# Optimization experiments

Measured on AMD Instinct MI355X. Metric: run time of the kernel, lower is better.

The kernel has to match this reference:

```python
import jax, jax.numpy as jnp
import numpy as np

B, S, H = 2, 2048, 768
NH, DH = 12, 64  # num_heads, dim_head; inner_dim = NH*DH = H
SCALE = DH ** -0.5


def setup_inputs() -> dict:
    key = jax.random.key(0)
    k1, k2, k3 = jax.random.split(key, 3)
    x = jax.random.normal(k1, (B, S, H), dtype=jnp.float32)
    w_qkv = jax.random.normal(k2, (3 * NH * DH, H), dtype=jnp.float32) * (H ** -0.5)
    w_out = jax.random.normal(k3, (H, NH * DH), dtype=jnp.float32) * ((NH * DH) ** -0.5)
    b_out = jnp.zeros((H,), dtype=jnp.float32)
    return {"x": x, "w_qkv": w_qkv, "w_out": w_out, "b_out": b_out}


def reference(x, w_qkv, w_out, b_out):
    b, s, _ = x.shape
    # qkv linear: [b, s, 3*inner]
    qkv = jnp.einsum('bsh,oh->bso', x, w_qkv)
    # 'b s (qkv l d) -> qkv b l s d'  (l = heads)
    qkv = qkv.reshape(b, s, 3, NH, DH).transpose(2, 0, 3, 1, 4)
    q, k, v = qkv[0], qkv[1], qkv[2]  # each [b, nh, s, dh]
    att = jax.nn.softmax(jnp.einsum('bhxd,bhyd->bhxy', q, k) * SCALE, axis=-1)
    out = jnp.einsum('bhxy,bhyd->bhxd', att, v)  # [b, nh, s, dh]
    out = out.transpose(0, 2, 1, 3).reshape(b, s, NH * DH)  # 'b h l d -> b l (h d)'
    return jnp.einsum('bsi,oi->bso', out, w_out) + b_out
```

## Files before the change

kernel.cpp:

```cpp
#include <hip/hip_runtime.h>
#include <cstdint>
#include <cstddef>

typedef __bf16 bf16;
typedef __bf16 bf16x8 __attribute__((ext_vector_type(8)));
typedef __bf16 bf16x4 __attribute__((ext_vector_type(4)));
typedef float  f32x4  __attribute__((ext_vector_type(4)));
typedef float  f32x16 __attribute__((ext_vector_type(16)));

constexpr int Bb  = 2;
constexpr int Ss  = 2048;
constexpr int Hh  = 768;
constexpr int NHh = 12;
constexpr int DHh = 64;
constexpr int Mm  = Bb * Ss;
constexpr int N3  = 3 * Hh;
constexpr int QKW = 2 * Hh;

__device__ __forceinline__ float fexp2(float x) { return __builtin_amdgcn_exp2f(x); }

__device__ __forceinline__ void gload_lds16(void* lds, const void* g) {
  __builtin_amdgcn_global_load_lds(
      (__attribute__((address_space(1))) void*)(uintptr_t)g,
      (__attribute__((address_space(3))) void*)(uint32_t)(uintptr_t)lds,
      16, 0, 0);
}

__global__ void cvt3_f32_bf16(const float* __restrict__ x,  bf16* __restrict__ xb,
                              const float* __restrict__ w1, bf16* __restrict__ w1b,
                              const float* __restrict__ w2, bf16* __restrict__ w2b) {
  const int st = gridDim.x * blockDim.x;
  int i0 = blockIdx.x * blockDim.x + threadIdx.x;
  for (int i = i0; i < 786432; i += st) {
    float4 v = ((const float4*)x)[i];
    bf16x4 o; o[0]=(bf16)v.x; o[1]=(bf16)v.y; o[2]=(bf16)v.z; o[3]=(bf16)v.w;
    ((bf16x4*)xb)[i] = o;
  }
  for (int i = i0; i < 442368; i += st) {
    float4 v = ((const float4*)w1)[i];
    bf16x4 o; o[0]=(bf16)v.x; o[1]=(bf16)v.y; o[2]=(bf16)v.z; o[3]=(bf16)v.w;
    ((bf16x4*)w1b)[i] = o;
  }
  for (int i = i0; i < 147456; i += st) {
    float4 v = ((const float4*)w2)[i];
    bf16x4 o; o[0]=(bf16)v.x; o[1]=(bf16)v.y; o[2]=(bf16)v.z; o[3]=(bf16)v.w;
    ((bf16x4*)w2b)[i] = o;
  }
}

template<int CSTRIDE, int OUTMODE, int BM>
__global__ __launch_bounds__(256, 2)
void gemm_bt(const bf16* __restrict__ A, const bf16* __restrict__ Bw,
             bf16* __restrict__ Cb, bf16* __restrict__ VtG,
             float* __restrict__ Cf, const float* __restrict__ bias)
{
  constexpr int K = 768;
  constexpr int NT = K / 32;
  constexpr int MI = BM / 32;
  constexpr int ABUF = BM * 64;
  __shared__ bf16 As[2][BM * 32];
  __shared__ bf16 Bs[2][128 * 32];
  const int tid  = threadIdx.x;
  const int wid  = tid >> 6, lane = tid & 63;
  const int lr   = lane & 15, lk = lane >> 4;
  const int n0   = blockIdx.x * 128, m0 = blockIdx.y * BM;
  const int wm   = (wid >> 1) * (BM / 2), wn = (wid & 1) * 64;

  f32x4 acc[MI][4] = {};

  const char* Ag = (const char*)(A  + (size_t)m0 * K) + (size_t)(tid >> 2) * (K * 2) + (tid & 3) * 16;
  const char* Bg = (const char*)(Bw + (size_t)n0 * K) + (size_t)(tid >> 2) * (K * 2) + (tid & 3) * 16;
  constexpr size_t rstep = (size_t)64 * K * 2;

  auto stage = [&](int buf, int kb) {
    char* aw = (char*)As + buf * ABUF + wid * 1024;
    char* bw = (char*)Bs + buf * 8192 + wid * 1024;
    gload_lds16(aw, Ag + (size_t)kb * 2);
    if constexpr (BM == 128)
      gload_lds16(aw + 4096, Ag + rstep + (size_t)kb * 2);
    gload_lds16(bw,        Bg + (size_t)kb * 2);
    gload_lds16(bw + 4096, Bg + rstep + (size_t)kb * 2);
  };

  stage(0, 0);
  asm volatile("s_waitcnt vmcnt(0)" ::: "memory");
  __syncthreads();

#pragma unroll 1
  for (int t = 0; t < NT; ++t) {
    const int cur = t & 1;
    if (t + 1 < NT) stage(cur ^ 1, (t + 1) * 32);
    __builtin_amdgcn_sched_barrier(0);

    bf16x8 af[MI], bfv[4];
#pragma unroll
    for (int i = 0; i < MI; ++i)
      af[i]  = *(const bf16x8*)((const char*)As + cur * ABUF + ((wm + i * 16 + lr) * 32 + lk * 8) * 2);
#pragma unroll
    for (int j = 0; j < 4; ++j)
      bfv[j] = *(const bf16x8*)((const char*)Bs + cur * 8192 + ((wn + j * 16 + lr) * 32 + lk * 8) * 2);
#pragma unroll
    for (int i = 0; i < MI; ++i)
#pragma unroll
      for (int j = 0; j < 4; ++j)
        acc[i][j] = __builtin_amdgcn_mfma_f32_16x16x32_bf16(af[i], bfv[j], acc[i][j], 0, 0, 0);

    __syncthreads();
  }

  if constexpr (OUTMODE == 1) {
#pragma unroll
    for (int i = 0; i < MI; ++i)
#pragma unroll
      for (int j = 0; j < 4; ++j) {
        const int n = n0 + wn + j * 16 + lr;
        const float bv = bias[n];
#pragma unroll
        for (int r = 0; r < 4; ++r) {
          const int m = m0 + wm + i * 16 + lk * 4 + r;
          Cf[(size_t)m * CSTRIDE + n] = acc[i][j][r] + bv;
        }
      }
  } else {
    if (n0 < QKW) {
#pragma unroll
      for (int i = 0; i < MI; ++i)
#pragma unroll
        for (int j = 0; j < 4; ++j) {
          const int n = n0 + wn + j * 16 + lr;
#pragma unroll
          for (int r = 0; r < 4; ++r) {
            const int m = m0 + wm + i * 16 + lk * 4 + r;
            Cb[(size_t)m * CSTRIDE + n] = (bf16)acc[i][j][r];
          }
        }
    } else {
      const int bidx = m0 >> 11;
      const int s0 = (m0 & 2047) + wm + lk * 4;
#pragma unroll
      for (int i = 0; i < MI; ++i)
#pragma unroll
        for (int j = 0; j < 4; ++j) {
          const int colv = (n0 - QKW) + wn + j * 16 + lr;
          const int hh = colv >> 6, dd = colv & 63;
          const int bh = bidx * NHh + hh;
          const int mb = s0 + i * 16;
          bf16x4 pv;
#pragma unroll
          for (int r = 0; r < 4; ++r) pv[r] = (bf16)acc[i][j][r];
          const size_t idx8 = (((size_t)bh * 128 + (mb >> 4)) * 2 + (dd >> 5)) * 64
                              + ((mb >> 3) & 1) * 32 + (dd & 31);
          *(bf16x4*)(VtG + idx8 * 8 + (mb & 7)) = pv;
        }
    }
  }
}

__global__ __launch_bounds__(256, 3)
void attn_fwd5(const bf16* __restrict__ qk, const bf16* __restrict__ Vfrag,
               bf16* __restrict__ aout)
{
  __shared__ __align__(16) char lds[32768];
  const int tid  = threadIdx.x;
  const int wid  = tid >> 6, lane = tid & 63;
  const int lq   = lane & 31, hi = lane >> 5;
  const int qh   = wid & 1, grp = wid >> 1;

  const int orig = blockIdx.x;
  const int swz  = (orig & 7) * 96 + (orig >> 3);
  const int qb   = swz & 31;
  const int bh   = swz >> 5;
  const int b    = bh / NHh, h = bh % NHh;
  const int q0   = qb * 64 + qh * 32;
  const int kvbase = grp * 1024;

  constexpr float Cs = 0.18033688011112042f;
  const bf16* qrow = qk + (size_t)(b * Ss + q0 + lq) * QKW + h * DHh;
  bf16x8 qf[4];
#pragma unroll
  for (int j = 0; j < 4; ++j) {
    bf16x8 t = *(const bf16x8*)(qrow + j * 16 + hi * 8);
#pragma unroll
    for (int e = 0; e < 8; ++e) t[e] = (bf16)((float)t[e] * Cs);
    qf[j] = t;
  }

  const int strow = qh * 32 + (lane >> 3);
  const int stcol = ((lane & 7) * 16) ^ (((lane >> 3) & 7) << 4);
  const char* Kg0 = (const char*)(qk + (size_t)(b * Ss) * QKW + Hh + h * DHh)
                    + (size_t)strow * (QKW * 2) + stcol;
  auto stageK = [&](int buf, int kvt) {
    char* db = lds + grp * 16384 + buf * 8192 + qh * 4096;
    const char* sg = Kg0 + (size_t)kvt * (QKW * 2);
#pragma unroll
    for (int c = 0; c < 4; ++c)
      gload_lds16(db + c * 1024, sg + (size_t)(c * 8) * (QKW * 2));
  };

  const char* Vf = (const char*)Vfrag + (size_t)bh * 262144 + lane * 16;

  f32x16 oacc[2] = {};
  f32x16 lacc = {};
  bf16x8 ones;
#pragma unroll
  for (int e = 0; e < 8; ++e) ones[e] = (bf16)1.0f;

  stageK(0, kvbase);
  asm volatile("s_waitcnt vmcnt(0)" ::: "memory");
  __builtin_amdgcn_sched_barrier(0);

#pragma unroll 1
  for (int i = 0; i < 16; ++i) {
    const int cur = i & 1;

    __builtin_amdgcn_s_barrier();

    bf16x8 vf[4][2];
    {
      const char* vp = Vf + (size_t)(grp * 64 + i * 4) * 2048;
#pragma unroll
      for (int s = 0; s < 4; ++s)
#pragma unroll
        for (int dc = 0; dc < 2; ++dc)
          vf[s][dc] = *(const bf16x8*)(vp + (s * 2 + dc) * 1024);
    }

    stageK(cur ^ 1, kvbase + ((i + 1) & 15) * 64);
    __builtin_amdgcn_sched_barrier(0);

    f32x16 sacc[2];
    __builtin_amdgcn_s_setprio(1);
#pragma unroll
    for (int kvc = 0; kvc < 2; ++kvc) {
      f32x16 s = {};
      const int row = kvc * 32 + lq;
      const char* kb = lds + grp * 16384 + cur * 8192 + row * 128;
      const int sw = (lq & 7) << 4;
#pragma unroll
      for (int j = 0; j < 4; ++j) {
        bf16x8 kf = *(const bf16x8*)(kb + ((j * 32 + hi * 16) ^ sw));
        s = __builtin_amdgcn_mfma_f32_32x32x16_bf16(kf, qf[j], s, 0, 0, 0);
      }
      sacc[kvc] = s;
    }
    __builtin_amdgcn_s_setprio(0);

    uint32_t w[2][8];
#pragma unroll
    for (int kvc = 0; kvc < 2; ++kvc)
#pragma unroll
      for (int m = 0; m < 8; ++m) {
        union { bf16 hh[2]; uint32_t u; } cv;
        cv.hh[0] = (bf16)fexp2(sacc[kvc][2 * m]);
        cv.hh[1] = (bf16)fexp2(sacc[kvc][2 * m + 1]);
        w[kvc][m] = cv.u;
      }

    asm volatile("s_waitcnt vmcnt(4)" ::: "memory");
    __builtin_amdgcn_sched_barrier(0);

    __builtin_amdgcn_s_setprio(1);
#pragma unroll
    for (int s = 0; s < 4; ++s) {
      const int kvc = s >> 1, sb = s & 1;
      uint32_t a0 = w[kvc][4 * sb + 0], b0 = w[kvc][4 * sb + 2];
      uint32_t a1 = w[kvc][4 * sb + 1], b1 = w[kvc][4 * sb + 3];
      asm("v_permlane32_swap_b32 %0, %1" : "+v"(a0), "+v"(b0));
      asm("v_permlane32_swap_b32 %0, %1" : "+v"(a1), "+v"(b1));
      union { uint32_t u[4]; bf16x8 v; } pf;
      pf.u[0] = a0; pf.u[1] = a1; pf.u[2] = b0; pf.u[3] = b1;
#pragma unroll
      for (int dc = 0; dc < 2; ++dc)
        oacc[dc] = __builtin_amdgcn_mfma_f32_32x32x16_bf16(vf[s][dc], pf.v, oacc[dc], 0, 0, 0);
      lacc = __builtin_amdgcn_mfma_f32_32x32x16_bf16(ones, pf.v, lacc, 0, 0, 0);
    }
    __builtin_amdgcn_s_setprio(0);

    asm volatile("s_waitcnt vmcnt(0)" ::: "memory");
    __builtin_amdgcn_sched_barrier(0);
  }

  __syncthreads();

  if (grp == 1) {
    char* mb = lds + qh * 8704;
#pragma unroll
    for (int dc = 0; dc < 2; ++dc)
#pragma unroll
      for (int rr = 0; rr < 4; ++rr) {
        f32x4 t;
#pragma unroll
        for (int e = 0; e < 4; ++e) t[e] = oacc[dc][rr * 4 + e];
        *(f32x4*)(mb + (dc * 4 + rr) * 1024 + lane * 16) = t;
      }
    *(float*)(mb + 8192 + lane * 4) = lacc[0];
  }
  __syncthreads();
  if (grp == 0) {
    const char* mb = lds + qh * 8704;
    const float l2 = *(const float*)(mb + 8192 + lane * 4);
    const float linv = 1.0f / (lacc[0] + l2);
    bf16* orow = aout + (size_t)(b * Ss + q0 + lq) * Hh + h * DHh;
#pragma unroll
    for (int dc = 0; dc < 2; ++dc)
#pragma unroll
      for (int rr = 0; rr < 4; ++rr) {
        const f32x4 o2 = *(const f32x4*)(mb + (dc * 4 + rr) * 1024 + lane * 16);
        bf16x4 ov;
#pragma unroll
        for (int e = 0; e < 4; ++e)
          ov[e] = (bf16)((oacc[dc][rr * 4 + e] + o2[e]) * linv);
        *(bf16x4*)(orow + dc * 32 + rr * 8 + hi * 4) = ov;
      }
  }
}

extern "C" void kernel_launch(void* const* d_in, const int* in_sizes, int n_in,
                              void* d_out, int out_size, void* d_ws, size_t ws_size,
                              hipStream_t stream) {
  const float* x     = (const float*)d_in[0];
  const float* w_qkv = (const float*)d_in[1];
  const float* w_out = (const float*)d_in[2];
  const float* b_out = (const float*)d_in[3];
  char* ws = (char*)d_ws;
  bf16* xb    = (bf16*)(ws + 0);
  bf16* wqkvb = (bf16*)(ws + 6291456);
  bf16* woutb = (bf16*)(ws + 9830400);
  bf16* qkb   = (bf16*)(ws + 11010048);
  bf16* Vfrag = (bf16*)(ws + 23592960);
  bf16* aoutb = (bf16*)(ws + 29884416);

  cvt3_f32_bf16<<<2048, 256, 0, stream>>>(x, xb, w_qkv, wqkvb, w_out, woutb);

  gemm_bt<QKW, 0, 128><<<dim3(18, 32), 256, 0, stream>>>(xb, wqkvb, qkb, Vfrag, nullptr, nullptr);
  attn_fwd5<<<768, 256, 0, stream>>>(qkb, Vfrag, aoutb);
  gemm_bt<Hh, 1, 64><<<dim3(6, 64), 256, 0, stream>>>(aoutb, woutb, nullptr, nullptr,
                                                      (float*)d_out, b_out);
}
```

Measured before the change: 87.90 us.

## Write K in MFMA fragment layout and load K/V straight to registers

The QKV GEMM epilogue now writes K into a per-head fragment layout that matches the MFMA operand order, as was already done for V. This lets the attention kernel drop LDS staging and block barriers for K and load K and V fragments directly into registers, prefetching the next tile after the PV step. The row-sum now comes from adding the exp values in registers rather than from an extra MFMA against a ones vector. LDS use shrinks and launch bounds go up to 4 blocks per CU. The trade-offs are scattered 2-byte stores in the GEMM epilogue for K and more registers held live for the prefetched fragments.

```diff
diff --git a/kernel.cpp b/kernel.cpp
--- a/kernel.cpp
+++ b/kernel.cpp
@@ -48,10 +48,10 @@
   }
 }
 
-template<int CSTRIDE, int OUTMODE, int BM>
+template<int OUTMODE, int BM>
 __global__ __launch_bounds__(256, 2)
 void gemm_bt(const bf16* __restrict__ A, const bf16* __restrict__ Bw,
-             bf16* __restrict__ Cb, bf16* __restrict__ VtG,
+             bf16* __restrict__ Qb, bf16* __restrict__ Kf, bf16* __restrict__ Vf,
              float* __restrict__ Cf, const float* __restrict__ bias)
 {
   constexpr int K = 768;
@@ -118,11 +118,13 @@
 #pragma unroll
         for (int r = 0; r < 4; ++r) {
           const int m = m0 + wm + i * 16 + lk * 4 + r;
-          Cf[(size_t)m * CSTRIDE + n] = acc[i][j][r] + bv;
+          Cf[(size_t)m * Hh + n] = acc[i][j][r] + bv;
         }
       }
   } else {
-    if (n0 < QKW) {
+    const int bidx = m0 >> 11;
+    const int kvb  = (m0 & 2047) + wm + lk * 4;
+    if (n0 < Hh) {
 #pragma unroll
       for (int i = 0; i < MI; ++i)
 #pragma unroll
@@ -131,12 +133,26 @@
 #pragma unroll
           for (int r = 0; r < 4; ++r) {
             const int m = m0 + wm + i * 16 + lk * 4 + r;
-            Cb[(size_t)m * CSTRIDE + n] = (bf16)acc[i][j][r];
+            Qb[(size_t)m * Hh + n] = (bf16)acc[i][j][r];
+          }
+        }
+    } else if (n0 < QKW) {
+#pragma unroll
+      for (int i = 0; i < MI; ++i)
+#pragma unroll
+        for (int j = 0; j < 4; ++j) {
+          const int colv = (n0 - Hh) + wn + j * 16 + lr;
+          const int hh = colv >> 6, dd = colv & 63;
+          bf16* kfh = Kf + (size_t)(bidx * NHh + hh) * 131072;
+#pragma unroll
+          for (int r = 0; r < 4; ++r) {
+            const int kv = kvb + i * 16 + r;
+            const size_t idx = (size_t)((((kv >> 5) * 4 + (dd >> 4)) * 64
+                                + ((dd >> 3) & 1) * 32 + (kv & 31)) * 8 + (dd & 7));
+            kfh[idx] = (bf16)acc[i][j][r];
           }
         }
     } else {
-      const int bidx = m0 >> 11;
-      const int s0 = (m0 & 2047) + wm + lk * 4;
 #pragma unroll
       for (int i = 0; i < MI; ++i)
 #pragma unroll
@@ -144,23 +160,23 @@
           const int colv = (n0 - QKW) + wn + j * 16 + lr;
           const int hh = colv >> 6, dd = colv & 63;
           const int bh = bidx * NHh + hh;
-          const int mb = s0 + i * 16;
+          const int mb = kvb + i * 16;
           bf16x4 pv;
 #pragma unroll
           for (int r = 0; r < 4; ++r) pv[r] = (bf16)acc[i][j][r];
           const size_t idx8 = (((size_t)bh * 128 + (mb >> 4)) * 2 + (dd >> 5)) * 64
                               + ((mb >> 3) & 1) * 32 + (dd & 31);
-          *(bf16x4*)(VtG + idx8 * 8 + (mb & 7)) = pv;
+          *(bf16x4*)(Vf + idx8 * 8 + (mb & 7)) = pv;
         }
     }
   }
 }
 
-__global__ __launch_bounds__(256, 3)
-void attn_fwd5(const bf16* __restrict__ qk, const bf16* __restrict__ Vfrag,
-               bf16* __restrict__ aout)
+__global__ __launch_bounds__(256, 4)
+void attn_fwd6(const bf16* __restrict__ Qb, const bf16* __restrict__ Kfrag,
+               const bf16* __restrict__ Vfrag, bf16* __restrict__ aout)
 {
-  __shared__ __align__(16) char lds[32768];
+  __shared__ __align__(16) char lds[17408];
   const int tid  = threadIdx.x;
   const int wid  = tid >> 6, lane = tid & 63;
   const int lq   = lane & 31, hi = lane >> 5;
@@ -172,10 +188,9 @@
   const int bh   = swz >> 5;
   const int b    = bh / NHh, h = bh % NHh;
   const int q0   = qb * 64 + qh * 32;
-  const int kvbase = grp * 1024;
 
   constexpr float Cs = 0.18033688011112042f;
-  const bf16* qrow = qk + (size_t)(b * Ss + q0 + lq) * QKW + h * DHh;
+  const bf16* qrow = Qb + (size_t)(b * Ss + q0 + lq) * Hh + h * DHh;
   bf16x8 qf[4];
 #pragma unroll
   for (int j = 0; j < 4; ++j) {
@@ -185,47 +200,27 @@
     qf[j] = t;
   }
 
-  const int strow = qh * 32 + (lane >> 3);
-  const int stcol = ((lane & 7) * 16) ^ (((lane >> 3) & 7) << 4);
-  const char* Kg0 = (const char*)(qk + (size_t)(b * Ss) * QKW + Hh + h * DHh)
-                    + (size_t)strow * (QKW * 2) + stcol;
-  auto stageK = [&](int buf, int kvt) {
-    char* db = lds + grp * 16384 + buf * 8192 + qh * 4096;
-    const char* sg = Kg0 + (size_t)kvt * (QKW * 2);
-#pragma unroll
-    for (int c = 0; c < 4; ++c)
-      gload_lds16(db + c * 1024, sg + (size_t)(c * 8) * (QKW * 2));
-  };
-
-  const char* Vf = (const char*)Vfrag + (size_t)bh * 262144 + lane * 16;
+  const char* Kf = (const char*)Kfrag + (size_t)bh * 262144 + grp * 131072 + lane * 16;
+  const char* Vf = (const char*)Vfrag + (size_t)bh * 262144 + grp * 131072 + lane * 16;
 
   f32x16 oacc[2] = {};
-  f32x16 lacc = {};
-  bf16x8 ones;
-#pragma unroll
-  for (int e = 0; e < 8; ++e) ones[e] = (bf16)1.0f;
-
-  stageK(0, kvbase);
-  asm volatile("s_waitcnt vmcnt(0)" ::: "memory");
-  __builtin_amdgcn_sched_barrier(0);
+  float rsum = 0.f;
+
+  bf16x8 kf[2][4], vf[4][2];
+#pragma unroll
+  for (int kvc = 0; kvc < 2; ++kvc)
+#pragma unroll
+    for (int j = 0; j < 4; ++j)
+      kf[kvc][j] = *(const bf16x8*)(Kf + kvc * 4096 + j * 1024);
+#pragma unroll
+  for (int s4 = 0; s4 < 4; ++s4)
+#pragma unroll
+    for (int dc = 0; dc < 2; ++dc)
+      vf[s4][dc] = *(const bf16x8*)(Vf + (s4 * 2 + dc) * 1024);
 
 #pragma unroll 1
   for (int i = 0; i < 16; ++i) {
-    const int cur = i & 1;
-
-    __builtin_amdgcn_s_barrier();
-
-    bf16x8 vf[4][2];
-    {
-      const char* vp = Vf + (size_t)(grp * 64 + i * 4) * 2048;
-#pragma unroll
-      for (int s = 0; s < 4; ++s)
-#pragma unroll
-        for (int dc = 0; dc < 2; ++dc)
-          vf[s][dc] = *(const bf16x8*)(vp + (s * 2 + dc) * 1024);
-    }
-
-    stageK(cur ^ 1, kvbase + ((i + 1) & 15) * 64);
+    asm volatile("s_waitcnt vmcnt(8)" ::: "memory");
     __builtin_amdgcn_sched_barrier(0);
 
     f32x16 sacc[2];
@@ -233,36 +228,36 @@
 #pragma unroll
     for (int kvc = 0; kvc < 2; ++kvc) {
       f32x16 s = {};
-      const int row = kvc * 32 + lq;
-      const char* kb = lds + grp * 16384 + cur * 8192 + row * 128;
-      const int sw = (lq & 7) << 4;
-#pragma unroll
-      for (int j = 0; j < 4; ++j) {
-        bf16x8 kf = *(const bf16x8*)(kb + ((j * 32 + hi * 16) ^ sw));
-        s = __builtin_amdgcn_mfma_f32_32x32x16_bf16(kf, qf[j], s, 0, 0, 0);
-      }
+#pragma unroll
+      for (int j = 0; j < 4; ++j)
+        s = __builtin_amdgcn_mfma_f32_32x32x16_bf16(kf[kvc][j], qf[j], s, 0, 0, 0);
       sacc[kvc] = s;
     }
     __builtin_amdgcn_s_setprio(0);
+    __builtin_amdgcn_sched_barrier(0);
 
     uint32_t w[2][8];
+    float rp[4] = {0.f, 0.f, 0.f, 0.f};
 #pragma unroll
     for (int kvc = 0; kvc < 2; ++kvc)
 #pragma unroll
       for (int m = 0; m < 8; ++m) {
+        const float e0 = fexp2(sacc[kvc][2 * m]);
+        const float e1 = fexp2(sacc[kvc][2 * m + 1]);
+        rp[m & 3] += e0 + e1;
         union { bf16 hh[2]; uint32_t u; } cv;
-        cv.hh[0] = (bf16)fexp2(sacc[kvc][2 * m]);
-        cv.hh[1] = (bf16)fexp2(sacc[kvc][2 * m + 1]);
+        cv.hh[0] = (bf16)e0; cv.hh[1] = (bf16)e1;
         w[kvc][m] = cv.u;
       }
-
-    asm volatile("s_waitcnt vmcnt(4)" ::: "memory");
+    rsum += (rp[0] + rp[1]) + (rp[2] + rp[3]);
+
+    asm volatile("s_waitcnt vmcnt(0)" ::: "memory");
     __builtin_amdgcn_sched_barrier(0);
 
     __builtin_amdgcn_s_setprio(1);
 #pragma unroll
-    for (int s = 0; s < 4; ++s) {
-      const int kvc = s >> 1, sb = s & 1;
+    for (int s4 = 0; s4 < 4; ++s4) {
+      const int kvc = s4 >> 1, sb = s4 & 1;
       uint32_t a0 = w[kvc][4 * sb + 0], b0 = w[kvc][4 * sb + 2];
       uint32_t a1 = w[kvc][4 * sb + 1], b1 = w[kvc][4 * sb + 3];
       asm("v_permlane32_swap_b32 %0, %1" : "+v"(a0), "+v"(b0));
@@ -271,14 +266,29 @@
       pf.u[0] = a0; pf.u[1] = a1; pf.u[2] = b0; pf.u[3] = b1;
 #pragma unroll
       for (int dc = 0; dc < 2; ++dc)
-        oacc[dc] = __builtin_amdgcn_mfma_f32_32x32x16_bf16(vf[s][dc], pf.v, oacc[dc], 0, 0, 0);
-      lacc = __builtin_amdgcn_mfma_f32_32x32x16_bf16(ones, pf.v, lacc, 0, 0, 0);
+        oacc[dc] = __builtin_amdgcn_mfma_f32_32x32x16_bf16(vf[s4][dc], pf.v, oacc[dc], 0, 0, 0);
     }
     __builtin_amdgcn_s_setprio(0);
-
-    asm volatile("s_waitcnt vmcnt(0)" ::: "memory");
-    __builtin_amdgcn_sched_barrier(0);
-  }
+    __builtin_amdgcn_sched_barrier(0);
+
+    {
+      const int nx = (i + 1) & 15;
+      const char* kp = Kf + nx * 8192;
+      const char* vp = Vf + nx * 8192;
+#pragma unroll
+      for (int kvc = 0; kvc < 2; ++kvc)
+#pragma unroll
+        for (int j = 0; j < 4; ++j)
+          kf[kvc][j] = *(const bf16x8*)(kp + kvc * 4096 + j * 1024);
+#pragma unroll
+      for (int s4 = 0; s4 < 4; ++s4)
+#pragma unroll
+        for (int dc = 0; dc < 2; ++dc)
+          vf[s4][dc] = *(const bf16x8*)(vp + (s4 * 2 + dc) * 1024);
+    }
+  }
+
+  rsum += __shfl_xor(rsum, 32, 64);
 
   __syncthreads();
 
@@ -293,13 +303,13 @@
         for (int e = 0; e < 4; ++e) t[e] = oacc[dc][rr * 4 + e];
         *(f32x4*)(mb + (dc * 4 + rr) * 1024 + lane * 16) = t;
       }
-    *(float*)(mb + 8192 + lane * 4) = lacc[0];
+    *(float*)(mb + 8192 + lane * 4) = rsum;
   }
   __syncthreads();
   if (grp == 0) {
     const char* mb = lds + qh * 8704;
     const float l2 = *(const float*)(mb + 8192 + lane * 4);
-    const float linv = 1.0f / (lacc[0] + l2);
+    const float linv = 1.0f / (rsum + l2);
     bf16* orow = aout + (size_t)(b * Ss + q0 + lq) * Hh + h * DHh;
 #pragma unroll
     for (int dc = 0; dc < 2; ++dc)
@@ -326,14 +336,16 @@
   bf16* xb    = (bf16*)(ws + 0);
   bf16* wqkvb = (bf16*)(ws + 6291456);
   bf16* woutb = (bf16*)(ws + 9830400);
-  bf16* qkb   = (bf16*)(ws + 11010048);
+  bf16* Qb    = (bf16*)(ws + 11010048);
+  bf16* Kfrag = (bf16*)(ws + 17301504);
   bf16* Vfrag = (bf16*)(ws + 23592960);
   bf16* aoutb = (bf16*)(ws + 29884416);
 
   cvt3_f32_bf16<<<2048, 256, 0, stream>>>(x, xb, w_qkv, wqkvb, w_out, woutb);
 
-  gemm_bt<QKW, 0, 128><<<dim3(18, 32), 256, 0, stream>>>(xb, wqkvb, qkb, Vfrag, nullptr, nullptr);
-  attn_fwd5<<<768, 256, 0, stream>>>(qkb, Vfrag, aoutb);
-  gemm_bt<Hh, 1, 64><<<dim3(6, 64), 256, 0, stream>>>(aoutb, woutb, nullptr, nullptr,
-                                                      (float*)d_out, b_out);
-}
+  gemm_bt<0, 128><<<dim3(18, 32), 256, 0, stream>>>(xb, wqkvb, Qb, Kfrag, Vfrag,
+                                                    nullptr, nullptr);
+  attn_fwd6<<<768, 256, 0, stream>>>(Qb, Kfrag, Vfrag, aoutb);
+  gemm_bt<1, 64><<<dim3(6, 64), 256, 0, stream>>>(aoutb, woutb, nullptr, nullptr, nullptr,
+                                                  (float*)d_out, b_out);
+}
```

After: 129.8 us. 47.6% more time.
